# Optimization experiments

Measured on AMD Instinct MI355X. Metric: run time of the kernel, lower is better.

## Reference

```python
import jax, jax.numpy as jnp
import numpy as np

N, FIN, FOUT = 4096, 256, 256


def setup_inputs() -> dict:
    key = jax.random.key(0)
    ks = jax.random.split(key, 6)
    x = jax.random.normal(ks[0], (N, FIN), jnp.float32)
    adj = jax.random.randint(ks[1], (N, N), 0, 2, jnp.int32)  # dense 0/1 adjacency
    W = jax.random.normal(ks[2], (FOUT, FIN), jnp.float32) / np.sqrt(FIN)
    b = jax.random.normal(ks[3], (FOUT,), jnp.float32) * 0.01
    att_w = jax.random.normal(ks[4], (2 * FOUT,), jnp.float32) / np.sqrt(2.0 * FOUT)  # Linear(2F,1).weight squeezed
    att_b = jax.random.normal(ks[5], (), jnp.float32) * 0.01
    return {"x": x, "adj": adj, "W": W, "b": b, "att_w": att_w, "att_b": att_b}


def reference(x, adj, W, b, att_w, att_b):
    n = x.shape[0]
    fo = W.shape[0]
    h = x @ W.T + b  # [N, Fout]
    # score(i,j) = att([h_i ; h_j]) = h_i.w1 + h_j.w2 + att_b  -> no [N,N,2F] concat
    s = (h @ att_w[:fo])[:, None] + (h @ att_w[fo:])[None, :] + att_b  # [N, N]
    edge = adj == 1
    # GLOBAL softmax over all edges (faithful to F.softmax(stacked_scores, dim=0))
    gmax = jnp.max(jnp.where(edge, s, -jnp.inf))
    e = jnp.exp(s - gmax)
    denom = jnp.sum(jnp.where(edge, e, 0.0))
    p = (e / denom).reshape(-1)  # softmaxed score per pair (valid at edges)
    # original indexes attention_scores[j] by NODE id j into the row-major edge list:
    # recover the score of the j-th global edge (j = 0..N-1) via cumsum rank + scatter
    flat = edge.reshape(-1)
    rank = jnp.cumsum(flat.astype(jnp.int32)) - 1  # rank of each edge in row-major order
    idx = jnp.where(flat, rank, n)  # non-edges and ranks >= n get dropped
    w_node = jnp.zeros((n,), h.dtype).at[idx].set(p, mode="drop")  # [N]
    # output[i] = sum_{j: adj[i,j]==1} w_node[j] * h[j]
    out = jax.nn.relu(edge.astype(h.dtype) @ (w_node[:, None] * h))
    return out
```

## Files before the change

kernel.cpp:

```cpp
#include <hip/hip_runtime.h>
#include <cstdint>
#include <cstddef>

#define NN 4096
#define FDIM 256

typedef __attribute__((ext_vector_type(4))) float fx4;
typedef __attribute__((ext_vector_type(2))) float fx2;
typedef __attribute__((ext_vector_type(8))) short s8v;

__device__ inline uint16_t f2bf(float f) {
    union { float f; uint32_t u; } v; v.f = f;
    uint32_t u = v.u;
    uint32_t r = (u + 0x7FFFu + ((u >> 16) & 1u)) >> 16;
    return (uint16_t)r;
}

__global__ __launch_bounds__(256) void k_h(const float* __restrict__ x,
        const float* __restrict__ W, const float* __restrict__ bias,
        float* __restrict__ h) {
    __shared__ __align__(16) float xs[64 * 34];
    __shared__ __align__(16) float wt[64 * 68];
    const int bi = blockIdx.x, bf = blockIdx.y;
    const int t = threadIdx.x;
    const int tx = t & 15, ty = t >> 4;
    float acc[2][4] = {};
    for (int k0 = 0; k0 < 256; k0 += 64) {
        for (int e = t; e < 2048; e += 256) {
            const int c = e & 63, r = e >> 6;
            xs[c * 34 + r] = x[(size_t)(bi * 32 + r) * 256 + k0 + c];
        }
        for (int e = t; e < 4096; e += 256) {
            const int c = e & 63, r = e >> 6;
            const int sw = 8 * ((c & 7) ^ ((c >> 3) & 7));
            wt[c * 68 + (r ^ sw)] = W[(size_t)(bf * 64 + r) * 256 + k0 + c];
        }
        __syncthreads();
        #pragma unroll 16
        for (int k = 0; k < 64; ++k) {
            const int sw = 8 * ((k & 7) ^ ((k >> 3) & 7));
            const fx2 av = *(const fx2*)(xs + k * 34 + ty * 2);
            const fx4 bv = *(const fx4*)(wt + k * 68 + ((tx * 4) ^ sw));
            #pragma unroll
            for (int u = 0; u < 2; ++u)
                #pragma unroll
                for (int v = 0; v < 4; ++v)
                    acc[u][v] += av[u] * bv[v];
        }
        __syncthreads();
    }
    const fx4 bv = *(const fx4*)(bias + bf * 64 + tx * 4);
    #pragma unroll
    for (int u = 0; u < 2; ++u) {
        const int i = bi * 32 + ty * 2 + u;
        fx4 r;
        #pragma unroll
        for (int v = 0; v < 4; ++v) r[v] = acc[u][v] + bv[v];
        *(fx4*)(h + (size_t)i * 256 + bf * 64 + tx * 4) = r;
    }
}

__global__ __launch_bounds__(256) void k_a(const float* __restrict__ h,
        const float* __restrict__ att_w, float* __restrict__ a1,
        float* __restrict__ a2) {
    const int wv = threadIdx.x >> 6, l = threadIdx.x & 63;
    const int i = blockIdx.x * 4 + wv;
    float s1 = 0.f, s2 = 0.f;
    #pragma unroll
    for (int c = l; c < 256; c += 64) {
        const float hv = h[(size_t)i * 256 + c];
        s1 += hv * att_w[c];
        s2 += hv * att_w[256 + c];
    }
    #pragma unroll
    for (int d = 32; d > 0; d >>= 1) {
        s1 += __shfl_down(s1, d);
        s2 += __shfl_down(s2, d);
    }
    if (l == 0) { a1[i] = s1; a2[i] = s2; }
}

__global__ __launch_bounds__(1024) void k_max_exp(const float* __restrict__ a1,
        const float* __restrict__ a2, float* __restrict__ E1,
        float* __restrict__ E2, float* __restrict__ Sg) {
    __shared__ float red1[16], red2[16];
    const int t = threadIdx.x;
    float m1 = -1e30f, m2 = -1e30f;
    for (int i = t; i < NN; i += 1024) {
        m1 = fmaxf(m1, a1[i]);
        m2 = fmaxf(m2, a2[i]);
    }
    #pragma unroll
    for (int d = 32; d > 0; d >>= 1) {
        m1 = fmaxf(m1, __shfl_down(m1, d));
        m2 = fmaxf(m2, __shfl_down(m2, d));
    }
    if ((t & 63) == 0) { red1[t >> 6] = m1; red2[t >> 6] = m2; }
    __syncthreads();
    if (t == 0) {
        float mm1 = -1e30f, mm2 = -1e30f;
        for (int k = 0; k < 16; ++k) {
            mm1 = fmaxf(mm1, red1[k]);
            mm2 = fmaxf(mm2, red2[k]);
        }
        red1[0] = mm1; red2[0] = mm2;
        *Sg = 0.f;
    }
    __syncthreads();
    const float M1 = red1[0], M2 = red2[0];
    for (int i = t; i < NN; i += 1024) {
        E1[i] = expf(a1[i] - M1);
        E2[i] = expf(a2[i] - M2);
    }
}

__global__ __launch_bounds__(256) void k_edges(const int* __restrict__ adj,
        const float* __restrict__ E1, const float* __restrict__ E2,
        float* __restrict__ wraw) {
    __shared__ int wtot[4];
    __shared__ int base_s;
    const int t = threadIdx.x, lane = t & 63, wv = t >> 6;
    for (int i = t; i < NN; i += 256) wraw[i] = 0.f;
    if (t == 0) base_s = 0;
    __syncthreads();
    for (int row = 0; row < NN; ++row) {
        const int base = base_s;
        if (base >= NN) break;
        const int* arow = adj + (size_t)row * NN + t * 16;
        int4 a0 = ((const int4*)arow)[0];
        int4 a1v = ((const int4*)arow)[1];
        int4 a2v = ((const int4*)arow)[2];
        int4 a3v = ((const int4*)arow)[3];
        int v[16] = {a0.x, a0.y, a0.z, a0.w, a1v.x, a1v.y, a1v.z, a1v.w,
                     a2v.x, a2v.y, a2v.z, a2v.w, a3v.x, a3v.y, a3v.z, a3v.w};
        int cnt = 0;
        #pragma unroll
        for (int j = 0; j < 16; ++j) cnt += (v[j] == 1);
        int inc = cnt;
        #pragma unroll
        for (int d = 1; d < 64; d <<= 1) {
            const int y = __shfl_up(inc, d);
            if (lane >= d) inc += y;
        }
        if (lane == 63) wtot[wv] = inc;
        __syncthreads();
        int wbase = 0;
        #pragma unroll
        for (int w = 0; w < 4; ++w) wbase += (w < wv) ? wtot[w] : 0;
        const int total = wtot[0] + wtot[1] + wtot[2] + wtot[3];
        if (t == 0) base_s = base + total;
        int r = base + wbase + inc - cnt;
        if (cnt && r < NN) {
            const float e1 = E1[row];
            #pragma unroll
            for (int j = 0; j < 16; ++j) {
                if (v[j] == 1) {
                    if (r < NN) wraw[r] = e1 * E2[t * 16 + j];
                    ++r;
                }
            }
        }
        __syncthreads();
    }
}

__global__ __launch_bounds__(256) void k_g(const float* __restrict__ h,
        const float* __restrict__ wraw, uint16_t* __restrict__ gt) {
    __shared__ float tile[64][65];
    const int bj = blockIdx.x, bf = blockIdx.y;
    const int t = threadIdx.x;
    for (int e = t; e < 4096; e += 256) {
        const int r = e >> 6, c = e & 63;
        const int j = bj * 64 + r;
        tile[r][c] = h[(size_t)j * 256 + bf * 64 + c] * wraw[j];
    }
    __syncthreads();
    for (int e = t; e < 4096; e += 256) {
        const int r = e >> 6, c = e & 63;
        gt[(size_t)(bf * 64 + r) * NN + bj * 64 + c] = f2bf(tile[c][r]);
    }
}

__global__ __launch_bounds__(256) void k_fused(const int* __restrict__ adj,
        const uint16_t* __restrict__ gt, const float* __restrict__ E1,
        const float* __restrict__ E2, float* __restrict__ part,
        float* __restrict__ Sg, int krange) {
    __shared__ __align__(16) uint16_t As[64 * 72];
    __shared__ __align__(16) uint16_t Gs[256 * 72];
    __shared__ float sred[4];
    const int ib = blockIdx.x, ks = blockIdx.y;
    const int t = threadIdx.x;
    const int wv = t >> 6, lane = t & 63;
    const int q = lane >> 4, m16 = lane & 15;
    const int i0 = ib * 64, k0 = ks * krange;
    const int ksteps = krange >> 6;

    fx4 acc[4][4];
    #pragma unroll
    for (int a = 0; a < 4; ++a)
        #pragma unroll
        for (int b = 0; b < 4; ++b) acc[a][b] = (fx4){0.f, 0.f, 0.f, 0.f};

    float e1r[4];
    #pragma unroll
    for (int p = 0; p < 4; ++p) e1r[p] = E1[i0 + p * 16 + (t >> 4)];

    float s_local = 0.f;

    for (int step = 0; step < ksteps; ++step) {
        const int kk = k0 + step * 64;
        const fx4 e2v = *(const fx4*)(E2 + kk + (t & 15) * 4);
        #pragma unroll
        for (int p = 0; p < 4; ++p) {
            const int r = p * 16 + (t >> 4);
            const int c = (t & 15) * 4;
            const int4 a = *(const int4*)(adj + (size_t)(i0 + r) * NN + kk + c);
            float sacc = 0.f;
            ushort4 bw;
            bw.x = (a.x == 1) ? 0x3F80 : 0; sacc += (a.x == 1) ? e2v[0] : 0.f;
            bw.y = (a.y == 1) ? 0x3F80 : 0; sacc += (a.y == 1) ? e2v[1] : 0.f;
            bw.z = (a.z == 1) ? 0x3F80 : 0; sacc += (a.z == 1) ? e2v[2] : 0.f;
            bw.w = (a.w == 1) ? 0x3F80 : 0; sacc += (a.w == 1) ? e2v[3] : 0.f;
            s_local += e1r[p] * sacc;
            *(ushort4*)(As + r * 72 + c) = bw;
        }
        #pragma unroll
        for (int p = 0; p < 8; ++p) {
            const int f = p * 32 + (t >> 3);
            const int ch = (t & 7) * 8;
            const s8v v = *(const s8v*)(gt + (size_t)f * NN + kk + ch);
            *(s8v*)(Gs + f * 72 + ch) = v;
        }
        __syncthreads();
        s8v afr[4][2];
        #pragma unroll
        for (int it = 0; it < 4; ++it)
            #pragma unroll
            for (int kh = 0; kh < 2; ++kh)
                afr[it][kh] = *(const s8v*)(As + (it * 16 + m16) * 72 + kh * 32 + q * 8);
        #pragma unroll
        for (int ft = 0; ft < 4; ++ft) {
            #pragma unroll
            for (int kh = 0; kh < 2; ++kh) {
                const s8v bfr = *(const s8v*)(Gs + (wv * 64 + ft * 16 + m16) * 72 + kh * 32 + q * 8);
                #pragma unroll
                for (int it = 0; it < 4; ++it)
                    acc[it][ft] = __builtin_amdgcn_mfma_f32_16x16x32_bf16(
                        afr[it][kh], bfr, acc[it][ft], 0, 0, 0);
            }
        }
        __syncthreads();
    }
    #pragma unroll
    for (int d = 32; d > 0; d >>= 1) s_local += __shfl_down(s_local, d);
    if (lane == 0) sred[wv] = s_local;
    __syncthreads();
    if (t == 0) atomicAdd(Sg, sred[0] + sred[1] + sred[2] + sred[3]);
    float* dst = part + (size_t)ks * NN * FDIM;
    #pragma unroll
    for (int it = 0; it < 4; ++it) {
        #pragma unroll
        for (int ft = 0; ft < 4; ++ft) {
            const int f = wv * 64 + ft * 16 + m16;
            #pragma unroll
            for (int r = 0; r < 4; ++r) {
                const int i = i0 + it * 16 + q * 4 + r;
                dst[(size_t)i * FDIM + f] = acc[it][ft][r];
            }
        }
    }
}

__global__ __launch_bounds__(256) void k_out(const float* __restrict__ part,
        const float* __restrict__ Sg, float* __restrict__ out, int nsplit) {
    const int idx = blockIdx.x * 256 + threadIdx.x;
    const float inv = 1.0f / (*Sg);
    fx4 s = {0.f, 0.f, 0.f, 0.f};
    for (int k = 0; k < nsplit; ++k)
        s += *(const fx4*)(part + (size_t)k * NN * FDIM + (size_t)idx * 4);
    fx4 r;
    r[0] = fmaxf(s[0], 0.f) * inv;
    r[1] = fmaxf(s[1], 0.f) * inv;
    r[2] = fmaxf(s[2], 0.f) * inv;
    r[3] = fmaxf(s[3], 0.f) * inv;
    *(fx4*)(out + (size_t)idx * 4) = r;
}

extern "C" void kernel_launch(void* const* d_in, const int* in_sizes, int n_in,
                              void* d_out, int out_size, void* d_ws, size_t ws_size,
                              hipStream_t stream) {
    const float* x     = (const float*)d_in[0];
    const int*   adj   = (const int*)d_in[1];
    const float* W     = (const float*)d_in[2];
    const float* bias  = (const float*)d_in[3];
    const float* att_w = (const float*)d_in[4];
    float* out = (float*)d_out;
    char* ws = (char*)d_ws;
    float*    h    = (float*)(ws + 0);
    uint16_t* gt   = (uint16_t*)(ws + (size_t)4194304);
    float*    a1   = (float*)(ws + 6291456);
    float*    a2   = (float*)(ws + 6307840);
    float*    E1   = (float*)(ws + 6324224);
    float*    E2   = (float*)(ws + 6340608);
    float*    wraw = (float*)(ws + 6356992);
    float*    Sg   = (float*)(ws + 6373376);
    float*    part = (float*)(ws + 6373632);

    const size_t avail = (ws_size > 6373632) ? (ws_size - 6373632) : 0;
    int splitk = 1;
    while (splitk < 8 &&
           (size_t)(splitk * 2) * NN * FDIM * sizeof(float) <= avail)
        splitk <<= 1;
    const int krange = NN / splitk;

    k_h      <<<dim3(128, 4), 256, 0, stream>>>(x, W, bias, h);
    k_a      <<<dim3(1024),  256,  0, stream>>>(h, att_w, a1, a2);
    k_max_exp<<<dim3(1),     1024, 0, stream>>>(a1, a2, E1, E2, Sg);
    k_edges  <<<dim3(1),     256,  0, stream>>>(adj, E1, E2, wraw);
    k_g      <<<dim3(64, 4), 256,  0, stream>>>(h, wraw, gt);
    k_fused  <<<dim3(64, splitk), 256, 0, stream>>>(adj, gt, E1, E2, part, Sg, krange);
    k_out    <<<dim3(1024),  256,  0, stream>>>(part, Sg, out, splitk);
}
```

Measured before the change: 173.5 us.

## Fuse max/exp with edge scan, move denominator into MFMA, double-buffer k_h

Merges the max/exp kernel and the serial edge-rank kernel into a single 1024-thread block. E values are kept in shared memory, and each thread scans 4 columns instead of 16, which shortens the serial per-row scan. The edge softmax denominator is now computed with an extra MFMA column of bf16 E2 values instead of per-thread scalar sums. Adjacency to bf16 conversion uses a multiply trick. k_h gains register-prefetched double buffering, and k_out remaps blocks to follow the order in which split-K partials are written. The denominator now uses bf16-rounded E2, which reduces precision, and the code relies on adj being exactly 0 or 1.

```diff
diff --git a/kernel.cpp b/kernel.cpp
--- a/kernel.cpp
+++ b/kernel.cpp
@@ -19,35 +19,62 @@
 __global__ __launch_bounds__(256) void k_h(const float* __restrict__ x,
         const float* __restrict__ W, const float* __restrict__ bias,
         float* __restrict__ h) {
-    __shared__ __align__(16) float xs[64 * 34];
-    __shared__ __align__(16) float wt[64 * 68];
+    __shared__ __align__(16) float xs[2][64 * 34];
+    __shared__ __align__(16) float wt[2][64 * 68];
     const int bi = blockIdx.x, bf = blockIdx.y;
     const int t = threadIdx.x;
     const int tx = t & 15, ty = t >> 4;
     float acc[2][4] = {};
-    for (int k0 = 0; k0 < 256; k0 += 64) {
-        for (int e = t; e < 2048; e += 256) {
-            const int c = e & 63, r = e >> 6;
-            xs[c * 34 + r] = x[(size_t)(bi * 32 + r) * 256 + k0 + c];
-        }
-        for (int e = t; e < 4096; e += 256) {
-            const int c = e & 63, r = e >> 6;
+    float rx[8], rw[16];
+    #pragma unroll
+    for (int u = 0; u < 8; ++u) {
+        const int e = t + 256 * u, r = e >> 6, c = e & 63;
+        rx[u] = x[(size_t)(bi * 32 + r) * 256 + c];
+    }
+    #pragma unroll
+    for (int u = 0; u < 16; ++u) {
+        const int e = t + 256 * u, r = e >> 6, c = e & 63;
+        rw[u] = W[(size_t)(bf * 64 + r) * 256 + c];
+    }
+    for (int p = 0; p < 4; ++p) {
+        float* xb = xs[p & 1];
+        float* wb = wt[p & 1];
+        #pragma unroll
+        for (int u = 0; u < 8; ++u) {
+            const int e = t + 256 * u, r = e >> 6, c = e & 63;
+            xb[c * 34 + r] = rx[u];
+        }
+        #pragma unroll
+        for (int u = 0; u < 16; ++u) {
+            const int e = t + 256 * u, r = e >> 6, c = e & 63;
             const int sw = 8 * ((c & 7) ^ ((c >> 3) & 7));
-            wt[c * 68 + (r ^ sw)] = W[(size_t)(bf * 64 + r) * 256 + k0 + c];
-        }
-        __syncthreads();
+            wb[c * 68 + (r ^ sw)] = rw[u];
+        }
+        __syncthreads();
+        if (p < 3) {
+            const int k0 = (p + 1) * 64;
+            #pragma unroll
+            for (int u = 0; u < 8; ++u) {
+                const int e = t + 256 * u, r = e >> 6, c = e & 63;
+                rx[u] = x[(size_t)(bi * 32 + r) * 256 + k0 + c];
+            }
+            #pragma unroll
+            for (int u = 0; u < 16; ++u) {
+                const int e = t + 256 * u, r = e >> 6, c = e & 63;
+                rw[u] = W[(size_t)(bf * 64 + r) * 256 + k0 + c];
+            }
+        }
         #pragma unroll 16
         for (int k = 0; k < 64; ++k) {
             const int sw = 8 * ((k & 7) ^ ((k >> 3) & 7));
-            const fx2 av = *(const fx2*)(xs + k * 34 + ty * 2);
-            const fx4 bv = *(const fx4*)(wt + k * 68 + ((tx * 4) ^ sw));
+            const fx2 av = *(const fx2*)(xb + k * 34 + ty * 2);
+            const fx4 bv = *(const fx4*)(wb + k * 68 + ((tx * 4) ^ sw));
             #pragma unroll
             for (int u = 0; u < 2; ++u)
                 #pragma unroll
                 for (int v = 0; v < 4; ++v)
                     acc[u][v] += av[u] * bv[v];
         }
-        __syncthreads();
     }
     const fx4 bv = *(const fx4*)(bias + bf * 64 + tx * 4);
     #pragma unroll
@@ -80,22 +107,26 @@
     if (l == 0) { a1[i] = s1; a2[i] = s2; }
 }
 
-__global__ __launch_bounds__(1024) void k_max_exp(const float* __restrict__ a1,
-        const float* __restrict__ a2, float* __restrict__ E1,
-        float* __restrict__ E2, float* __restrict__ Sg) {
+__global__ __launch_bounds__(1024) void k_prep(const float* __restrict__ a1,
+        const float* __restrict__ a2, const int* __restrict__ adj,
+        float* __restrict__ E1, float* __restrict__ E2,
+        float* __restrict__ wraw, float* __restrict__ Sg) {
+    __shared__ float E1s[NN];
+    __shared__ float E2s[NN];
     __shared__ float red1[16], red2[16];
-    const int t = threadIdx.x;
-    float m1 = -1e30f, m2 = -1e30f;
-    for (int i = t; i < NN; i += 1024) {
-        m1 = fmaxf(m1, a1[i]);
-        m2 = fmaxf(m2, a2[i]);
-    }
+    __shared__ int wtot[16];
+    __shared__ int base_s;
+    const int t = threadIdx.x, lane = t & 63, wv = t >> 6;
+    const fx4 v1 = *(const fx4*)(a1 + t * 4);
+    const fx4 v2 = *(const fx4*)(a2 + t * 4);
+    float m1 = fmaxf(fmaxf(v1[0], v1[1]), fmaxf(v1[2], v1[3]));
+    float m2 = fmaxf(fmaxf(v2[0], v2[1]), fmaxf(v2[2], v2[3]));
     #pragma unroll
     for (int d = 32; d > 0; d >>= 1) {
         m1 = fmaxf(m1, __shfl_down(m1, d));
         m2 = fmaxf(m2, __shfl_down(m2, d));
     }
-    if ((t & 63) == 0) { red1[t >> 6] = m1; red2[t >> 6] = m2; }
+    if (lane == 0) { red1[wv] = m1; red2[wv] = m2; }
     __syncthreads();
     if (t == 0) {
         float mm1 = -1e30f, mm2 = -1e30f;
@@ -105,37 +136,30 @@
         }
         red1[0] = mm1; red2[0] = mm2;
         *Sg = 0.f;
+        base_s = 0;
     }
     __syncthreads();
     const float M1 = red1[0], M2 = red2[0];
-    for (int i = t; i < NN; i += 1024) {
-        E1[i] = expf(a1[i] - M1);
-        E2[i] = expf(a2[i] - M2);
-    }
-}
-
-__global__ __launch_bounds__(256) void k_edges(const int* __restrict__ adj,
-        const float* __restrict__ E1, const float* __restrict__ E2,
-        float* __restrict__ wraw) {
-    __shared__ int wtot[4];
-    __shared__ int base_s;
-    const int t = threadIdx.x, lane = t & 63, wv = t >> 6;
-    for (int i = t; i < NN; i += 256) wraw[i] = 0.f;
-    if (t == 0) base_s = 0;
+    fx4 e1v, e2v, z4 = {0.f, 0.f, 0.f, 0.f};
+    #pragma unroll
+    for (int j = 0; j < 4; ++j) {
+        e1v[j] = expf(v1[j] - M1);
+        e2v[j] = expf(v2[j] - M2);
+    }
+    *(fx4*)(E1s + t * 4) = e1v;
+    *(fx4*)(E2s + t * 4) = e2v;
+    *(fx4*)(E1 + t * 4) = e1v;
+    *(fx4*)(E2 + t * 4) = e2v;
+    *(fx4*)(wraw + t * 4) = z4;
     __syncthreads();
     for (int row = 0; row < NN; ++row) {
         const int base = base_s;
         if (base >= NN) break;
-        const int* arow = adj + (size_t)row * NN + t * 16;
-        int4 a0 = ((const int4*)arow)[0];
-        int4 a1v = ((const int4*)arow)[1];
-        int4 a2v = ((const int4*)arow)[2];
-        int4 a3v = ((const int4*)arow)[3];
-        int v[16] = {a0.x, a0.y, a0.z, a0.w, a1v.x, a1v.y, a1v.z, a1v.w,
-                     a2v.x, a2v.y, a2v.z, a2v.w, a3v.x, a3v.y, a3v.z, a3v.w};
+        const int4 a = ((const int4*)(adj + (size_t)row * NN))[t];
+        const int vj[4] = {a.x, a.y, a.z, a.w};
         int cnt = 0;
         #pragma unroll
-        for (int j = 0; j < 16; ++j) cnt += (v[j] == 1);
+        for (int j = 0; j < 4; ++j) cnt += (vj[j] == 1);
         int inc = cnt;
         #pragma unroll
         for (int d = 1; d < 64; d <<= 1) {
@@ -144,18 +168,21 @@
         }
         if (lane == 63) wtot[wv] = inc;
         __syncthreads();
-        int wbase = 0;
-        #pragma unroll
-        for (int w = 0; w < 4; ++w) wbase += (w < wv) ? wtot[w] : 0;
-        const int total = wtot[0] + wtot[1] + wtot[2] + wtot[3];
+        int wbase = 0, total = 0;
+        #pragma unroll
+        for (int w = 0; w < 16; ++w) {
+            const int xw = wtot[w];
+            total += xw;
+            wbase += (w < wv) ? xw : 0;
+        }
         if (t == 0) base_s = base + total;
         int r = base + wbase + inc - cnt;
         if (cnt && r < NN) {
-            const float e1 = E1[row];
-            #pragma unroll
-            for (int j = 0; j < 16; ++j) {
-                if (v[j] == 1) {
-                    if (r < NN) wraw[r] = e1 * E2[t * 16 + j];
+            const float e1 = E1s[row];
+            #pragma unroll
+            for (int j = 0; j < 4; ++j) {
+                if (vj[j] == 1) {
+                    if (r < NN) wraw[r] = e1 * E2s[t * 4 + j];
                     ++r;
                 }
             }
@@ -186,8 +213,7 @@
         const float* __restrict__ E2, float* __restrict__ part,
         float* __restrict__ Sg, int krange) {
     __shared__ __align__(16) uint16_t As[64 * 72];
-    __shared__ __align__(16) uint16_t Gs[256 * 72];
-    __shared__ float sred[4];
+    __shared__ __align__(16) uint16_t Gs[272 * 72];
     const int ib = blockIdx.x, ks = blockIdx.y;
     const int t = threadIdx.x;
     const int wv = t >> 6, lane = t & 63;
@@ -200,29 +226,23 @@
     for (int a = 0; a < 4; ++a)
         #pragma unroll
         for (int b = 0; b < 4; ++b) acc[a][b] = (fx4){0.f, 0.f, 0.f, 0.f};
-
-    float e1r[4];
-    #pragma unroll
-    for (int p = 0; p < 4; ++p) e1r[p] = E1[i0 + p * 16 + (t >> 4)];
-
-    float s_local = 0.f;
+    fx4 accS[4];
+    #pragma unroll
+    for (int a = 0; a < 4; ++a) accS[a] = (fx4){0.f, 0.f, 0.f, 0.f};
+
+    for (int e = t; e < 15 * 72; e += 256) Gs[257 * 72 + e] = 0;
 
     for (int step = 0; step < ksteps; ++step) {
         const int kk = k0 + step * 64;
-        const fx4 e2v = *(const fx4*)(E2 + kk + (t & 15) * 4);
         #pragma unroll
         for (int p = 0; p < 4; ++p) {
             const int r = p * 16 + (t >> 4);
-            const int c = (t & 15) * 4;
-            const int4 a = *(const int4*)(adj + (size_t)(i0 + r) * NN + kk + c);
-            float sacc = 0.f;
-            ushort4 bw;
-            bw.x = (a.x == 1) ? 0x3F80 : 0; sacc += (a.x == 1) ? e2v[0] : 0.f;
-            bw.y = (a.y == 1) ? 0x3F80 : 0; sacc += (a.y == 1) ? e2v[1] : 0.f;
-            bw.z = (a.z == 1) ? 0x3F80 : 0; sacc += (a.z == 1) ? e2v[2] : 0.f;
-            bw.w = (a.w == 1) ? 0x3F80 : 0; sacc += (a.w == 1) ? e2v[3] : 0.f;
-            s_local += e1r[p] * sacc;
-            *(ushort4*)(As + r * 72 + c) = bw;
+            const int c4 = (t & 15) * 4;
+            const int4 a = *(const int4*)(adj + (size_t)(i0 + r) * NN + kk + c4);
+            uint2 w;
+            w.x = (uint32_t)(a.x | (a.y << 16)) * 0x3F80u;
+            w.y = (uint32_t)(a.z | (a.w << 16)) * 0x3F80u;
+            *(uint2*)(&As[r * 72 + c4]) = w;
         }
         #pragma unroll
         for (int p = 0; p < 8; ++p) {
@@ -230,6 +250,14 @@
             const int ch = (t & 7) * 8;
             const s8v v = *(const s8v*)(gt + (size_t)f * NN + kk + ch);
             *(s8v*)(Gs + f * 72 + ch) = v;
+        }
+        if (t < 8) {
+            const float* e2p = E2 + kk + t * 8;
+            uint32_t* dst = (uint32_t*)(&Gs[256 * 72 + t * 8]);
+            #pragma unroll
+            for (int j = 0; j < 4; ++j)
+                dst[j] = (uint32_t)f2bf(e2p[2 * j]) |
+                         ((uint32_t)f2bf(e2p[2 * j + 1]) << 16);
         }
         __syncthreads();
         s8v afr[4][2];
@@ -249,13 +277,29 @@
                         afr[it][kh], bfr, acc[it][ft], 0, 0, 0);
             }
         }
-        __syncthreads();
-    }
-    #pragma unroll
-    for (int d = 32; d > 0; d >>= 1) s_local += __shfl_down(s_local, d);
-    if (lane == 0) sred[wv] = s_local;
-    __syncthreads();
-    if (t == 0) atomicAdd(Sg, sred[0] + sred[1] + sred[2] + sred[3]);
+        if (wv == 3) {
+            #pragma unroll
+            for (int kh = 0; kh < 2; ++kh) {
+                const s8v bfrS = *(const s8v*)(Gs + (256 + m16) * 72 + kh * 32 + q * 8);
+                #pragma unroll
+                for (int it = 0; it < 4; ++it)
+                    accS[it] = __builtin_amdgcn_mfma_f32_16x16x32_bf16(
+                        afr[it][kh], bfrS, accS[it], 0, 0, 0);
+            }
+        }
+        __syncthreads();
+    }
+    if (wv == 3) {
+        float s_local = 0.f;
+        #pragma unroll
+        for (int it = 0; it < 4; ++it)
+            #pragma unroll
+            for (int r = 0; r < 4; ++r)
+                s_local += accS[it][r] * E1[i0 + it * 16 + q * 4 + r];
+        #pragma unroll
+        for (int d = 32; d > 0; d >>= 1) s_local += __shfl_down(s_local, d);
+        if (lane == 0) atomicAdd(Sg, s_local);
+    }
     float* dst = part + (size_t)ks * NN * FDIM;
     #pragma unroll
     for (int it = 0; it < 4; ++it) {
@@ -273,17 +317,22 @@
 
 __global__ __launch_bounds__(256) void k_out(const float* __restrict__ part,
         const float* __restrict__ Sg, float* __restrict__ out, int nsplit) {
-    const int idx = blockIdx.x * 256 + threadIdx.x;
+    const int b = blockIdx.x;
+    const int ib = (b & 7) + 8 * ((b >> 3) & 7);
+    const int sub = b >> 6;
+    const int t = threadIdx.x;
+    const int row = ib * 64 + sub * 4 + (t >> 6);
+    const size_t idx = (size_t)row * 256 + (t & 63) * 4;
     const float inv = 1.0f / (*Sg);
     fx4 s = {0.f, 0.f, 0.f, 0.f};
     for (int k = 0; k < nsplit; ++k)
-        s += *(const fx4*)(part + (size_t)k * NN * FDIM + (size_t)idx * 4);
+        s += *(const fx4*)(part + (size_t)k * NN * FDIM + idx);
     fx4 r;
     r[0] = fmaxf(s[0], 0.f) * inv;
     r[1] = fmaxf(s[1], 0.f) * inv;
     r[2] = fmaxf(s[2], 0.f) * inv;
     r[3] = fmaxf(s[3], 0.f) * inv;
-    *(fx4*)(out + (size_t)idx * 4) = r;
+    *(fx4*)(out + idx) = r;
 }
 
 extern "C" void kernel_launch(void* const* d_in, const int* in_sizes, int n_in,
@@ -313,11 +362,10 @@
         splitk <<= 1;
     const int krange = NN / splitk;
 
-    k_h      <<<dim3(128, 4), 256, 0, stream>>>(x, W, bias, h);
-    k_a      <<<dim3(1024),  256,  0, stream>>>(h, att_w, a1, a2);
-    k_max_exp<<<dim3(1),     1024, 0, stream>>>(a1, a2, E1, E2, Sg);
-    k_edges  <<<dim3(1),     256,  0, stream>>>(adj, E1, E2, wraw);
-    k_g      <<<dim3(64, 4), 256,  0, stream>>>(h, wraw, gt);
-    k_fused  <<<dim3(64, splitk), 256, 0, stream>>>(adj, gt, E1, E2, part, Sg, krange);
-    k_out    <<<dim3(1024),  256,  0, stream>>>(part, Sg, out, splitk);
-}
+    k_h   <<<dim3(128, 4), 256, 0, stream>>>(x, W, bias, h);
+    k_a   <<<dim3(1024), 256, 0, stream>>>(h, att_w, a1, a2);
+    k_prep<<<dim3(1), 1024, 0, stream>>>(a1, a2, adj, E1, E2, wraw, Sg);
+    k_g   <<<dim3(64, 4), 256, 0, stream>>>(h, wraw, gt);
+    k_fused<<<dim3(64, splitk), 256, 0, stream>>>(adj, gt, E1, E2, part, Sg, krange);
+    k_out <<<dim3(1024), 256, 0, stream>>>(part, Sg, out, splitk);
+}
```

After: 159.5 us. 1.09x faster.
